# Kernel optimization log

Hardware: AMD Instinct MI355X
Metric: run time of the kernel (lower is better)

The kernel has to match this reference:

```python
import jax, jax.numpy as jnp
import numpy as np

T, D_IN, H, D_OUT = 20, 4, 768, 1
B = 1024


def setup_inputs() -> dict:
    key = jax.random.key(0)
    ks = jax.random.split(key, 8)
    s = 1.0 / np.sqrt(H)
    return {
        "batch_price": jax.random.normal(ks[0], (B, T, D_IN), jnp.float32),
        "batch_event": jax.random.normal(ks[1], (B, T, H), jnp.float32),
        "W_ih": jax.random.uniform(ks[2], (T, 4 * H, D_IN), jnp.float32, -s, s),
        "W_hh": jax.random.uniform(ks[3], (T, 4 * H, H), jnp.float32, -s, s),
        "b_ih": jax.random.uniform(ks[4], (T, 4 * H), jnp.float32, -s, s),
        "b_hh": jax.random.uniform(ks[5], (T, 4 * H), jnp.float32, -s, s),
        "fc_w": jax.random.uniform(ks[6], (D_OUT, H), jnp.float32, -s, s),
        "fc_b": jax.random.uniform(ks[7], (D_OUT,), jnp.float32, -s, s),
    }


def _lstm_cell(x, h_mat, c, wih, whh, bih, bhh):
    # gates: [B, 4H] in PyTorch LSTMCell order (i, f, g, o)
    gates = x @ wih.T + bih + h_mat @ whh.T + bhh
    i, f, g, o = jnp.split(gates, 4, axis=-1)
    c_next = jax.nn.sigmoid(f) * c + jax.nn.sigmoid(i) * jnp.tanh(g)
    h_next = jax.nn.sigmoid(o) * jnp.tanh(c_next)
    return h_next, c_next


def reference(batch_price, batch_event, W_ih, W_hh, b_ih, b_hh, fc_w, fc_b):
    Bb, Tt, _ = batch_price.shape
    Hh = W_hh.shape[-1]
    # step 0: hx = batch_event[:, 0], cell state = zeros
    h, c = _lstm_cell(batch_price[:, 0], batch_event[:, 0],
                      jnp.zeros((Bb, Hh), batch_price.dtype),
                      W_ih[0], W_hh[0], b_ih[0], b_hh[0])

    def step(carry, inp):
        h, c = carry
        x, ev, wih, whh, bih, bhh = inp
        # faithful to source: hx = torch.sum(batch_event_t + h_prev) -> scalar
        hx = jnp.sum(ev + h)
        h_mat = jnp.broadcast_to(hx, (Bb, Hh))
        h2, c2 = _lstm_cell(x, h_mat, c, wih, whh, bih, bhh)
        return (h2, c2), None

    xs = (jnp.swapaxes(batch_price[:, 1:], 0, 1),  # [T-1, B, D_IN]
          jnp.swapaxes(batch_event[:, 1:], 0, 1),  # [T-1, B, H]
          W_ih[1:], W_hh[1:], b_ih[1:], b_hh[1:])
    (h, c), _ = jax.lax.scan(step, (h, c), xs)
    return h @ fc_w.T + fc_b  # [B, 1]
```

## Files before the change

kernel.cpp:

```cpp
#include <hip/hip_runtime.h>
#include <stdint.h>

#define Bsz 1024
#define Tn  20
#define Hn  768
#define G4n 3072

#define WS_SH    0
#define WS_SEV   32
#define WS_PART  64
#define WS_BCAST 576
#define WS_RS    640
#define WS_BS    (640 + Tn*G4n)
#define WS_C     (640 + 2*Tn*G4n)

#define NB_GEMM   768
#define NB_ROWSUM 14592
#define NB_BIAS   240
#define NB_SEV    1216
#define NB_TOTAL  (NB_GEMM + NB_ROWSUM + NB_BIAS + NB_SEV)

typedef float  floatx4 __attribute__((ext_vector_type(4)));
typedef short  bfrag8  __attribute__((ext_vector_type(8)));

__device__ __forceinline__ float wave_reduce(float v){
#pragma unroll
    for (int o = 32; o > 0; o >>= 1) v += __shfl_down(v, o, 64);
    return v;
}
__device__ __forceinline__ float sigf(float x){ return 1.0f/(1.0f+__expf(-x)); }
__device__ __forceinline__ float tanhfast(float x){ return 2.0f/(1.0f+__expf(-2.0f*x)) - 1.0f; }
__device__ __forceinline__ unsigned short f2bf(float f){
    uint32_t u = __float_as_uint(f);
    return (unsigned short)((u + 0x7fffu + ((u>>16)&1u)) >> 16);
}
__device__ __forceinline__ float bf2f(unsigned short h){ return __uint_as_float(((uint32_t)h)<<16); }
__device__ __forceinline__ uint64_t pack_tv(unsigned t, float v){
    return ((uint64_t)t << 32) | (uint64_t)__float_as_uint(v);
}

__global__ void k_init(float* __restrict__ ws){
    if (threadIdx.x < 640) ws[threadIdx.x] = 0.0f;
}

__global__ __launch_bounds__(256) void k_pre(
    const float* __restrict__ price, const float* __restrict__ ev,
    const float* __restrict__ wih,   const float* __restrict__ whh,
    const float* __restrict__ bih,   const float* __restrict__ bhh,
    float* __restrict__ ws)
{
    __shared__ __align__(16) char smraw[4*64*56*2 + 16];
    unsigned short* Ah = (unsigned short*)smraw;
    unsigned short* Al = Ah + 64*56;
    unsigned short* Bh = Al + 64*56;
    unsigned short* Bl = Bh + 64*56;
    float* redk = (float*)(smraw + 4*64*56*2);
    float* red  = (float*)smraw;

    int blk = blockIdx.x, tid = threadIdx.x;

    if (blk < NB_GEMM) {
        float* Sh   = ws + WS_SH;
        float* cbuf = ws + WS_C;
        int bt = blk / 48, kt = blk % 48;
        int b0 = bt*64, k0 = kt*16;
        int w = tid >> 6, lane = tid & 63;
        int q = lane >> 4, col = lane & 15;

        int srow = tid >> 2;
        int kkoff = (tid & 3) * 8;
        int g_s = srow >> 4, rr = srow & 15;
        const float* aRow = ev  + (size_t)(b0 + srow)*(Tn*Hn);
        const float* bRow = whh + (size_t)(g_s*Hn + k0 + rr)*Hn;

        floatx4 acc[4];
#pragma unroll
        for (int g = 0; g < 4; ++g) acc[g] = (floatx4){0.f,0.f,0.f,0.f};

        for (int kk0 = 0; kk0 < Hn; kk0 += 32) {
            {
                const float* p = aRow + kk0 + kkoff;
                float4 v0 = *(const float4*)p;
                float4 v1 = *(const float4*)(p+4);
                float f[8] = {v0.x,v0.y,v0.z,v0.w,v1.x,v1.y,v1.z,v1.w};
                bfrag8 hv, lv;
#pragma unroll
                for (int i = 0; i < 8; ++i) {
                    unsigned short hb = f2bf(f[i]);
                    hv[i] = (short)hb;
                    lv[i] = (short)f2bf(f[i] - bf2f(hb));
                }
                *(bfrag8*)&Ah[srow*56 + kkoff] = hv;
                *(bfrag8*)&Al[srow*56 + kkoff] = lv;
                const float* pb = bRow + kk0 + kkoff;
                float4 u0 = *(const float4*)pb;
                float4 u1 = *(const float4*)(pb+4);
                float fb[8] = {u0.x,u0.y,u0.z,u0.w,u1.x,u1.y,u1.z,u1.w};
#pragma unroll
                for (int i = 0; i < 8; ++i) {
                    unsigned short hb = f2bf(fb[i]);
                    hv[i] = (short)hb;
                    lv[i] = (short)f2bf(fb[i] - bf2f(hb));
                }
                *(bfrag8*)&Bh[srow*56 + kkoff] = hv;
                *(bfrag8*)&Bl[srow*56 + kkoff] = lv;
            }
            __syncthreads();

            bfrag8 ah = *(const bfrag8*)&Ah[(w*16 + col)*56 + q*8];
            bfrag8 al = *(const bfrag8*)&Al[(w*16 + col)*56 + q*8];
#pragma unroll
            for (int g = 0; g < 4; ++g) {
                bfrag8 bh = *(const bfrag8*)&Bh[(g*16 + col)*56 + q*8];
                bfrag8 bl = *(const bfrag8*)&Bl[(g*16 + col)*56 + q*8];
                acc[g] = __builtin_amdgcn_mfma_f32_16x16x32_bf16(ah, bh, acc[g], 0,0,0);
                acc[g] = __builtin_amdgcn_mfma_f32_16x16x32_bf16(ah, bl, acc[g], 0,0,0);
                acc[g] = __builtin_amdgcn_mfma_f32_16x16x32_bf16(al, bh, acc[g], 0,0,0);
            }
            __syncthreads();
        }

        float hsum = 0.f;
#pragma unroll
        for (int r = 0; r < 4; ++r) {
            int b = b0 + w*16 + q*4 + r;
            float4 xv = *(const float4*)(price + (size_t)b*(Tn*4));
            float gates[4];
#pragma unroll
            for (int g = 0; g < 4; ++g) {
                int j = g*Hn + k0 + col;
                float4 wv = *(const float4*)(wih + (size_t)j*4);
                gates[g] = acc[g][r] + xv.x*wv.x + xv.y*wv.y + xv.z*wv.z + xv.w*wv.w
                         + bih[j] + bhh[j];
            }
            float c0 = sigf(gates[0]) * tanhfast(gates[2]);
            float h0 = sigf(gates[3]) * tanhfast(c0);
            cbuf[(size_t)b*Hn + k0 + col] = c0;
            hsum += h0;
        }
        hsum = wave_reduce(hsum);
        if (lane == 0) redk[w] = hsum;
        __syncthreads();
        if (tid == 0) atomicAdd(&Sh[0], redk[0]+redk[1]+redk[2]+redk[3]);
        return;
    }

    blk -= NB_GEMM;
    float* Sev     = ws + WS_SEV;
    float* rowsum  = ws + WS_RS;
    float* biassum = ws + WS_BS;

    if (blk < NB_ROWSUM) {
        int r    = blk*4 + (tid>>6);
        int lane = tid & 63;
        int t    = 1 + r/G4n;
        int j    = r - (t-1)*G4n;
        const float* base = whh + (size_t)t*G4n*Hn + (size_t)j*Hn;
        float s = 0.f;
#pragma unroll
        for (int i = 0; i < 3; ++i) {
            float4 v = *(const float4*)(base + (size_t)(lane + 64*i)*4);
            s += v.x + v.y + v.z + v.w;
        }
        s = wave_reduce(s);
        if (lane == 0) rowsum[t*G4n + j] = s;
    } else if (blk < NB_ROWSUM + NB_BIAS) {
        int idx = (blk - NB_ROWSUM)*256 + tid;
        if (idx < Tn*G4n) biassum[idx] = bih[idx] + bhh[idx];
    } else {
        int sb = blk - NB_ROWSUM - NB_BIAS;
        int t  = 1 + (sb >> 6);
        int b0 = (sb & 63) * 16;
        float s = 0.f;
        for (int bb = 0; bb < 16; ++bb) {
            const float* base = ev + (size_t)(b0+bb)*(Tn*Hn) + (size_t)t*Hn;
            s += base[tid] + base[tid+256] + base[tid+512];
        }
        s = wave_reduce(s);
        if ((tid & 63) == 0) red[tid>>6] = s;
        __syncthreads();
        if (tid == 0) atomicAdd(&Sev[t], red[0]+red[1]+red[2]+red[3]);
    }
}

__global__ __launch_bounds__(768) void k_steps(
    const float* __restrict__ price, const float* __restrict__ wih,
    const float* __restrict__ fcw,   const float* __restrict__ fcb,
    float* __restrict__ ws, float* __restrict__ out)
{
    __shared__ float pr[4][80];
    __shared__ float red[12];
    __shared__ float redP[4];
    __shared__ float redF[4][12];
    __shared__ float shx;

    float* Sh  = ws + WS_SH;
    float* Sev = ws + WS_SEV;
    uint64_t* part  = (uint64_t*)(ws + WS_PART);
    uint64_t* bcast = (uint64_t*)(ws + WS_BCAST);
    const float* rowsum  = ws + WS_RS;
    const float* biassum = ws + WS_BS;
    float* cbuf = ws + WS_C;

    int blk = blockIdx.x, tid = threadIdx.x;
    int lane = tid & 63, wid = tid >> 6;
    int k = tid;

    if (tid < 320) {
        int e = tid / 80, r = tid - e*80;
        pr[e][r] = price[(size_t)(blk + 256*e)*(Tn*4) + r];
    }

    float c[4];
#pragma unroll
    for (int e = 0; e < 4; ++e)
        c[e] = cbuf[(size_t)(blk + 256*e)*Hn + k];

    float fcwk = fcw[k];
    float fcb0 = fcb[0];

    float hsum_prev = 0.f;
    float vout[4] = {0.f,0.f,0.f,0.f};

    for (int t = 1; t < Tn; ++t) {
        const float* wih_t = wih + (size_t)t*G4n*4;
        float rsv[4], base[4][4];
#pragma unroll
        for (int g = 0; g < 4; ++g) {
            int j = g*Hn + k;
            float4 wv = *(const float4*)(wih_t + (size_t)j*4);
            rsv[g]   = rowsum[t*G4n + j];
            float bs = biassum[t*G4n + j];
#pragma unroll
            for (int e = 0; e < 4; ++e) {
                base[e][g] = pr[e][t*4+0]*wv.x + pr[e][t*4+1]*wv.y
                           + pr[e][t*4+2]*wv.z + pr[e][t*4+3]*wv.w + bs;
            }
        }

        if (t >= 2) {
            float v = wave_reduce(hsum_prev);
            if (lane == 0) red[wid] = v;
            __syncthreads();
            if (tid == 0) {
                float tot = 0.f;
#pragma unroll
                for (int i = 0; i < 12; ++i) tot += red[i];
                __hip_atomic_store(&part[blk], pack_tv((unsigned)(t-1), tot),
                                   __ATOMIC_RELAXED, __HIP_MEMORY_SCOPE_AGENT);
            }
        }

        if (blk == 0) {
            if (t >= 2) {
                if (tid < 256) {
                    uint64_t u;
                    do { u = __hip_atomic_load(&part[tid], __ATOMIC_RELAXED, __HIP_MEMORY_SCOPE_AGENT); }
                    while ((unsigned)(u >> 32) != (unsigned)(t-1));
                    float pv = wave_reduce(__uint_as_float((uint32_t)u));
                    if (lane == 0) redP[wid] = pv;
                }
                __syncthreads();
                if (tid == 0) {
                    float Shprev = redP[0]+redP[1]+redP[2]+redP[3];
                    float hx = Sev[t] + Shprev;
                    shx = hx;
                    __hip_atomic_store(bcast, pack_tv((unsigned)t, hx),
                                       __ATOMIC_RELAXED, __HIP_MEMORY_SCOPE_AGENT);
                }
            } else {
                if (tid == 0) {
                    float hx = Sev[1] + Sh[0];
                    shx = hx;
                    __hip_atomic_store(bcast, pack_tv(1u, hx),
                                       __ATOMIC_RELAXED, __HIP_MEMORY_SCOPE_AGENT);
                }
            }
            __syncthreads();
        } else {
            if (tid == 0) {
                uint64_t u;
                do { u = __hip_atomic_load(bcast, __ATOMIC_RELAXED, __HIP_MEMORY_SCOPE_AGENT); }
                while ((unsigned)(u >> 32) != (unsigned)t);
                shx = __uint_as_float((uint32_t)u);
            }
            __syncthreads();
        }
        float hx = shx;

        float hsum = 0.f;
#pragma unroll
        for (int e = 0; e < 4; ++e) {
            float gi = base[e][0] + hx*rsv[0];
            float gf = base[e][1] + hx*rsv[1];
            float gg = base[e][2] + hx*rsv[2];
            float go = base[e][3] + hx*rsv[3];
            float cn = sigf(gf)*c[e] + sigf(gi)*tanhfast(gg);
            c[e] = cn;
            float h = sigf(go)*tanhfast(cn);
            hsum += h;
            if (t == Tn-1) vout[e] = wave_reduce(h * fcwk);
        }
        hsum_prev = hsum;
    }

    if (lane == 0) {
#pragma unroll
        for (int e = 0; e < 4; ++e) redF[e][wid] = vout[e];
    }
    __syncthreads();
    if (tid < 4) {
        float tot = 0.f;
#pragma unroll
        for (int i = 0; i < 12; ++i) tot += redF[tid][i];
        out[blk + 256*tid] = tot + fcb0;
    }
}

extern "C" void kernel_launch(void* const* d_in, const int* in_sizes, int n_in,
                              void* d_out, int out_size, void* d_ws, size_t ws_size,
                              hipStream_t stream)
{
    const float* price = (const float*)d_in[0];
    const float* ev    = (const float*)d_in[1];
    const float* wih   = (const float*)d_in[2];
    const float* whh   = (const float*)d_in[3];
    const float* bih   = (const float*)d_in[4];
    const float* bhh   = (const float*)d_in[5];
    const float* fcw   = (const float*)d_in[6];
    const float* fcb   = (const float*)d_in[7];
    float* out = (float*)d_out;
    float* ws  = (float*)d_ws;

    k_init<<<1, 640, 0, stream>>>(ws);
    k_pre <<<NB_TOTAL, 256, 0, stream>>>(price, ev, wih, whh, bih, bhh, ws);
    k_steps<<<256, 768, 0, stream>>>(price, wih, fcw, fcb, ws, out);
}
```

Before: 416.4 us.

## Pre-split bf16 operands, skip forget gate, widen reductions, decentralize step sync

Adds a conversion kernel that splits the event slice and recurrent weights into bf16 hi/lo once, so the step-0 GEMM reads them straight from global memory without the LDS staging and syncthreads. That GEMM drops the forget-gate columns, since the initial cell state is zero. Row-sum and event-sum reductions each handle eight rows per wave with float4 loads, and the bias sum is vectorised. In the step kernel every block polls all partial sums directly, with a sleep, instead of waiting for block 0 to broadcast, which removes one global hop per step but adds polling traffic.

Result: slower. 475.2 us (+14.1%).

```diff
diff --git a/kernel.cpp b/kernel.cpp
--- a/kernel.cpp
+++ b/kernel.cpp
@@ -11,14 +11,23 @@
 #define WS_PART  64
 #define WS_BCAST 576
 #define WS_RS    640
-#define WS_BS    (640 + Tn*G4n)
-#define WS_C     (640 + 2*Tn*G4n)
+#define WS_BS    62080
+#define WS_C     123520
+#define WS_EVH   909952
+#define WS_EVL   1303168
+#define WS_WH    1696384
+#define WS_WL    2581120
+
+#define NBC_EV   512
+#define NBC_W    1152
+#define NBC_Z    3
+#define NBC_TOT  (NBC_EV + NBC_W + NBC_Z)
 
 #define NB_GEMM   768
-#define NB_ROWSUM 14592
-#define NB_BIAS   240
-#define NB_SEV    1216
-#define NB_TOTAL  (NB_GEMM + NB_ROWSUM + NB_BIAS + NB_SEV)
+#define NB_ROWSUM 1824
+#define NB_SEV    608
+#define NB_BIAS   60
+#define NB_TOTAL  (NB_GEMM + NB_ROWSUM + NB_SEV + NB_BIAS)
 
 typedef float  floatx4 __attribute__((ext_vector_type(4)));
 typedef short  bfrag8  __attribute__((ext_vector_type(8)));
@@ -39,8 +48,47 @@
     return ((uint64_t)t << 32) | (uint64_t)__float_as_uint(v);
 }
 
-__global__ void k_init(float* __restrict__ ws){
-    if (threadIdx.x < 640) ws[threadIdx.x] = 0.0f;
+__global__ __launch_bounds__(256) void k_conv(
+    const float* __restrict__ ev, const float* __restrict__ whh,
+    float* __restrict__ ws)
+{
+    int bid = blockIdx.x, tid = threadIdx.x;
+    if (bid < NBC_EV + NBC_W) {
+        if (tid >= 192) return;
+        int r = tid / 96;
+        int i = (tid - r*96) * 8;
+        const float* src;
+        unsigned short *dh, *dl;
+        if (bid < NBC_EV) {
+            int b = bid*2 + r;
+            src = ev + (size_t)b*(Tn*Hn) + i;
+            dh = (unsigned short*)(ws + WS_EVH) + (size_t)b*Hn + i;
+            dl = (unsigned short*)(ws + WS_EVL) + (size_t)b*Hn + i;
+        } else {
+            int p = (bid - NBC_EV)*2 + r;
+            int gsel = p / Hn;
+            int ga = (gsel==0) ? 0 : (gsel==1 ? 2 : 3);
+            int j = ga*Hn + (p - gsel*Hn);
+            src = whh + (size_t)j*Hn + i;
+            dh = (unsigned short*)(ws + WS_WH) + (size_t)p*Hn + i;
+            dl = (unsigned short*)(ws + WS_WL) + (size_t)p*Hn + i;
+        }
+        float4 v0 = *(const float4*)src;
+        float4 v1 = *(const float4*)(src+4);
+        float f[8] = {v0.x,v0.y,v0.z,v0.w,v1.x,v1.y,v1.z,v1.w};
+        bfrag8 hv, lv;
+#pragma unroll
+        for (int q = 0; q < 8; ++q) {
+            unsigned short hb = f2bf(f[q]);
+            hv[q] = (short)hb;
+            lv[q] = (short)f2bf(f[q] - bf2f(hb));
+        }
+        *(bfrag8*)dh = hv;
+        *(bfrag8*)dl = lv;
+    } else {
+        int idx = (bid - NBC_EV - NBC_W)*256 + tid;
+        if (idx < 640) ws[idx] = 0.0f;
+    }
 }
 
 __global__ __launch_bounds__(256) void k_pre(
@@ -49,75 +97,58 @@
     const float* __restrict__ bih,   const float* __restrict__ bhh,
     float* __restrict__ ws)
 {
-    __shared__ __align__(16) char smraw[4*64*56*2 + 16];
-    unsigned short* Ah = (unsigned short*)smraw;
-    unsigned short* Al = Ah + 64*56;
-    unsigned short* Bh = Al + 64*56;
-    unsigned short* Bl = Bh + 64*56;
-    float* redk = (float*)(smraw + 4*64*56*2);
-    float* red  = (float*)smraw;
-
+    __shared__ float redk[4];
     int blk = blockIdx.x, tid = threadIdx.x;
+    int lane = tid & 63, wid = tid >> 6;
 
     if (blk < NB_GEMM) {
         float* Sh   = ws + WS_SH;
         float* cbuf = ws + WS_C;
         int bt = blk / 48, kt = blk % 48;
         int b0 = bt*64, k0 = kt*16;
-        int w = tid >> 6, lane = tid & 63;
-        int q = lane >> 4, col = lane & 15;
-
-        int srow = tid >> 2;
-        int kkoff = (tid & 3) * 8;
-        int g_s = srow >> 4, rr = srow & 15;
-        const float* aRow = ev  + (size_t)(b0 + srow)*(Tn*Hn);
-        const float* bRow = whh + (size_t)(g_s*Hn + k0 + rr)*Hn;
-
-        floatx4 acc[4];
-#pragma unroll
-        for (int g = 0; g < 4; ++g) acc[g] = (floatx4){0.f,0.f,0.f,0.f};
-
-        for (int kk0 = 0; kk0 < Hn; kk0 += 32) {
-            {
-                const float* p = aRow + kk0 + kkoff;
-                float4 v0 = *(const float4*)p;
-                float4 v1 = *(const float4*)(p+4);
-                float f[8] = {v0.x,v0.y,v0.z,v0.w,v1.x,v1.y,v1.z,v1.w};
-                bfrag8 hv, lv;
-#pragma unroll
-                for (int i = 0; i < 8; ++i) {
-                    unsigned short hb = f2bf(f[i]);
-                    hv[i] = (short)hb;
-                    lv[i] = (short)f2bf(f[i] - bf2f(hb));
-                }
-                *(bfrag8*)&Ah[srow*56 + kkoff] = hv;
-                *(bfrag8*)&Al[srow*56 + kkoff] = lv;
-                const float* pb = bRow + kk0 + kkoff;
-                float4 u0 = *(const float4*)pb;
-                float4 u1 = *(const float4*)(pb+4);
-                float fb[8] = {u0.x,u0.y,u0.z,u0.w,u1.x,u1.y,u1.z,u1.w};
-#pragma unroll
-                for (int i = 0; i < 8; ++i) {
-                    unsigned short hb = f2bf(fb[i]);
-                    hv[i] = (short)hb;
-                    lv[i] = (short)f2bf(fb[i] - bf2f(hb));
-                }
-                *(bfrag8*)&Bh[srow*56 + kkoff] = hv;
-                *(bfrag8*)&Bl[srow*56 + kkoff] = lv;
-            }
-            __syncthreads();
-
-            bfrag8 ah = *(const bfrag8*)&Ah[(w*16 + col)*56 + q*8];
-            bfrag8 al = *(const bfrag8*)&Al[(w*16 + col)*56 + q*8];
-#pragma unroll
-            for (int g = 0; g < 4; ++g) {
-                bfrag8 bh = *(const bfrag8*)&Bh[(g*16 + col)*56 + q*8];
-                bfrag8 bl = *(const bfrag8*)&Bl[(g*16 + col)*56 + q*8];
-                acc[g] = __builtin_amdgcn_mfma_f32_16x16x32_bf16(ah, bh, acc[g], 0,0,0);
-                acc[g] = __builtin_amdgcn_mfma_f32_16x16x32_bf16(ah, bl, acc[g], 0,0,0);
-                acc[g] = __builtin_amdgcn_mfma_f32_16x16x32_bf16(al, bh, acc[g], 0,0,0);
-            }
-            __syncthreads();
+        int w = wid, q = lane >> 4, col = lane & 15;
+
+        const unsigned short* evh = (const unsigned short*)(ws + WS_EVH);
+        const unsigned short* evl = (const unsigned short*)(ws + WS_EVL);
+        const unsigned short* wh  = (const unsigned short*)(ws + WS_WH);
+        const unsigned short* wl  = (const unsigned short*)(ws + WS_WL);
+
+        int arow = b0 + w*16 + col;
+        const unsigned short* pah = evh + (size_t)arow*Hn + q*8;
+        const unsigned short* pal = evl + (size_t)arow*Hn + q*8;
+        int br0 = 0*Hn + k0 + col;
+        int br1 = 1*Hn + k0 + col;
+        int br2 = 2*Hn + k0 + col;
+        const unsigned short* pbh0 = wh + (size_t)br0*Hn + q*8;
+        const unsigned short* pbl0 = wl + (size_t)br0*Hn + q*8;
+        const unsigned short* pbh1 = wh + (size_t)br1*Hn + q*8;
+        const unsigned short* pbl1 = wl + (size_t)br1*Hn + q*8;
+        const unsigned short* pbh2 = wh + (size_t)br2*Hn + q*8;
+        const unsigned short* pbl2 = wl + (size_t)br2*Hn + q*8;
+
+        floatx4 acc0 = (floatx4){0.f,0.f,0.f,0.f};
+        floatx4 acc1 = (floatx4){0.f,0.f,0.f,0.f};
+        floatx4 acc2 = (floatx4){0.f,0.f,0.f,0.f};
+
+#pragma unroll 4
+        for (int kk = 0; kk < Hn; kk += 32) {
+            bfrag8 ah = *(const bfrag8*)(pah + kk);
+            bfrag8 al = *(const bfrag8*)(pal + kk);
+            bfrag8 b0h = *(const bfrag8*)(pbh0 + kk);
+            bfrag8 b0l = *(const bfrag8*)(pbl0 + kk);
+            acc0 = __builtin_amdgcn_mfma_f32_16x16x32_bf16(ah, b0h, acc0, 0,0,0);
+            acc0 = __builtin_amdgcn_mfma_f32_16x16x32_bf16(ah, b0l, acc0, 0,0,0);
+            acc0 = __builtin_amdgcn_mfma_f32_16x16x32_bf16(al, b0h, acc0, 0,0,0);
+            bfrag8 b1h = *(const bfrag8*)(pbh1 + kk);
+            bfrag8 b1l = *(const bfrag8*)(pbl1 + kk);
+            acc1 = __builtin_amdgcn_mfma_f32_16x16x32_bf16(ah, b1h, acc1, 0,0,0);
+            acc1 = __builtin_amdgcn_mfma_f32_16x16x32_bf16(ah, b1l, acc1, 0,0,0);
+            acc1 = __builtin_amdgcn_mfma_f32_16x16x32_bf16(al, b1h, acc1, 0,0,0);
+            bfrag8 b2h = *(const bfrag8*)(pbh2 + kk);
+            bfrag8 b2l = *(const bfrag8*)(pbl2 + kk);
+            acc2 = __builtin_amdgcn_mfma_f32_16x16x32_bf16(ah, b2h, acc2, 0,0,0);
+            acc2 = __builtin_amdgcn_mfma_f32_16x16x32_bf16(ah, b2l, acc2, 0,0,0);
+            acc2 = __builtin_amdgcn_mfma_f32_16x16x32_bf16(al, b2h, acc2, 0,0,0);
         }
 
         float hsum = 0.f;
@@ -125,16 +156,17 @@
         for (int r = 0; r < 4; ++r) {
             int b = b0 + w*16 + q*4 + r;
             float4 xv = *(const float4*)(price + (size_t)b*(Tn*4));
-            float gates[4];
-#pragma unroll
-            for (int g = 0; g < 4; ++g) {
-                int j = g*Hn + k0 + col;
-                float4 wv = *(const float4*)(wih + (size_t)j*4);
-                gates[g] = acc[g][r] + xv.x*wv.x + xv.y*wv.y + xv.z*wv.z + xv.w*wv.w
-                         + bih[j] + bhh[j];
-            }
-            float c0 = sigf(gates[0]) * tanhfast(gates[2]);
-            float h0 = sigf(gates[3]) * tanhfast(c0);
+            int j0 = 0*Hn + k0 + col;
+            int j1 = 2*Hn + k0 + col;
+            int j2 = 3*Hn + k0 + col;
+            float4 w0 = *(const float4*)(wih + (size_t)j0*4);
+            float4 w1 = *(const float4*)(wih + (size_t)j1*4);
+            float4 w2 = *(const float4*)(wih + (size_t)j2*4);
+            float gi = acc0[r] + xv.x*w0.x + xv.y*w0.y + xv.z*w0.z + xv.w*w0.w + bih[j0] + bhh[j0];
+            float gg = acc1[r] + xv.x*w1.x + xv.y*w1.y + xv.z*w1.z + xv.w*w1.w + bih[j1] + bhh[j1];
+            float go = acc2[r] + xv.x*w2.x + xv.y*w2.y + xv.z*w2.z + xv.w*w2.w + bih[j2] + bhh[j2];
+            float c0 = sigf(gi) * tanhfast(gg);
+            float h0 = sigf(go) * tanhfast(c0);
             cbuf[(size_t)b*Hn + k0 + col] = c0;
             hsum += h0;
         }
@@ -146,40 +178,54 @@
     }
 
     blk -= NB_GEMM;
-    float* Sev     = ws + WS_SEV;
-    float* rowsum  = ws + WS_RS;
-    float* biassum = ws + WS_BS;
-
     if (blk < NB_ROWSUM) {
-        int r    = blk*4 + (tid>>6);
-        int lane = tid & 63;
-        int t    = 1 + r/G4n;
-        int j    = r - (t-1)*G4n;
-        const float* base = whh + (size_t)t*G4n*Hn + (size_t)j*Hn;
+        int gw = blk*4 + wid;
+        int t  = 1 + gw/384;
+        int j0 = (gw - (t-1)*384)*8;
+        const float* base = whh + ((size_t)t*G4n + j0)*Hn + (size_t)lane*4;
+        float s[8];
+#pragma unroll
+        for (int r = 0; r < 8; ++r) {
+            float4 v0 = *(const float4*)(base + (size_t)r*Hn);
+            float4 v1 = *(const float4*)(base + (size_t)r*Hn + 256);
+            float4 v2 = *(const float4*)(base + (size_t)r*Hn + 512);
+            s[r] = (v0.x+v0.y+v0.z+v0.w) + (v1.x+v1.y+v1.z+v1.w) + (v2.x+v2.y+v2.z+v2.w);
+        }
+        float* rowsum = ws + WS_RS;
+#pragma unroll
+        for (int r = 0; r < 8; ++r) {
+            float rs = wave_reduce(s[r]);
+            if (lane == 0) rowsum[(size_t)t*G4n + j0 + r] = rs;
+        }
+        return;
+    }
+
+    blk -= NB_ROWSUM;
+    if (blk < NB_SEV) {
+        int gw = blk*4 + wid;
+        int t   = 1 + gw/128;
+        int b0s = (gw - (t-1)*128)*8;
         float s = 0.f;
 #pragma unroll
-        for (int i = 0; i < 3; ++i) {
-            float4 v = *(const float4*)(base + (size_t)(lane + 64*i)*4);
-            s += v.x + v.y + v.z + v.w;
+        for (int r = 0; r < 8; ++r) {
+            const float* base = ev + ((size_t)(b0s+r)*Tn + t)*Hn + (size_t)lane*4;
+            float4 v0 = *(const float4*)(base);
+            float4 v1 = *(const float4*)(base + 256);
+            float4 v2 = *(const float4*)(base + 512);
+            s += (v0.x+v0.y+v0.z+v0.w) + (v1.x+v1.y+v1.z+v1.w) + (v2.x+v2.y+v2.z+v2.w);
         }
         s = wave_reduce(s);
-        if (lane == 0) rowsum[t*G4n + j] = s;
-    } else if (blk < NB_ROWSUM + NB_BIAS) {
-        int idx = (blk - NB_ROWSUM)*256 + tid;
-        if (idx < Tn*G4n) biassum[idx] = bih[idx] + bhh[idx];
-    } else {
-        int sb = blk - NB_ROWSUM - NB_BIAS;
-        int t  = 1 + (sb >> 6);
-        int b0 = (sb & 63) * 16;
-        float s = 0.f;
-        for (int bb = 0; bb < 16; ++bb) {
-            const float* base = ev + (size_t)(b0+bb)*(Tn*Hn) + (size_t)t*Hn;
-            s += base[tid] + base[tid+256] + base[tid+512];
-        }
-        s = wave_reduce(s);
-        if ((tid & 63) == 0) red[tid>>6] = s;
-        __syncthreads();
-        if (tid == 0) atomicAdd(&Sev[t], red[0]+red[1]+red[2]+red[3]);
+        if (lane == 0) atomicAdd(ws + WS_SEV + t, s);
+        return;
+    }
+
+    blk -= NB_SEV;
+    {
+        int idx = blk*256 + tid;
+        float4 a = *(const float4*)(bih + (size_t)idx*4);
+        float4 b = *(const float4*)(bhh + (size_t)idx*4);
+        float4 r4; r4.x=a.x+b.x; r4.y=a.y+b.y; r4.z=a.z+b.z; r4.w=a.w+b.w;
+        *(float4*)(ws + WS_BS + (size_t)idx*4) = r4;
     }
 }
 
@@ -192,12 +238,10 @@
     __shared__ float red[12];
     __shared__ float redP[4];
     __shared__ float redF[4][12];
-    __shared__ float shx;
 
     float* Sh  = ws + WS_SH;
     float* Sev = ws + WS_SEV;
-    uint64_t* part  = (uint64_t*)(ws + WS_PART);
-    uint64_t* bcast = (uint64_t*)(ws + WS_BCAST);
+    uint64_t* part = (uint64_t*)(ws + WS_PART);
     const float* rowsum  = ws + WS_RS;
     const float* biassum = ws + WS_BS;
     float* cbuf = ws + WS_C;
@@ -218,26 +262,14 @@
 
     float fcwk = fcw[k];
     float fcb0 = fcb[0];
+    float sh0  = Sh[0];
+
+    __syncthreads();
 
     float hsum_prev = 0.f;
     float vout[4] = {0.f,0.f,0.f,0.f};
 
     for (int t = 1; t < Tn; ++t) {
-        const float* wih_t = wih + (size_t)t*G4n*4;
-        float rsv[4], base[4][4];
-#pragma unroll
-        for (int g = 0; g < 4; ++g) {
-            int j = g*Hn + k;
-            float4 wv = *(const float4*)(wih_t + (size_t)j*4);
-            rsv[g]   = rowsum[t*G4n + j];
-            float bs = biassum[t*G4n + j];
-#pragma unroll
-            for (int e = 0; e < 4; ++e) {
-                base[e][g] = pr[e][t*4+0]*wv.x + pr[e][t*4+1]*wv.y
-                           + pr[e][t*4+2]*wv.z + pr[e][t*4+3]*wv.w + bs;
-            }
-        }
-
         if (t >= 2) {
             float v = wave_reduce(hsum_prev);
             if (lane == 0) red[wid] = v;
@@ -251,42 +283,38 @@
             }
         }
 
-        if (blk == 0) {
-            if (t >= 2) {
-                if (tid < 256) {
-                    uint64_t u;
-                    do { u = __hip_atomic_load(&part[tid], __ATOMIC_RELAXED, __HIP_MEMORY_SCOPE_AGENT); }
-                    while ((unsigned)(u >> 32) != (unsigned)(t-1));
-                    float pv = wave_reduce(__uint_as_float((uint32_t)u));
-                    if (lane == 0) redP[wid] = pv;
+        const float* wih_t = wih + (size_t)t*G4n*4;
+        float rsv[4], base[4][4];
+#pragma unroll
+        for (int g = 0; g < 4; ++g) {
+            int j = g*Hn + k;
+            float4 wv = *(const float4*)(wih_t + (size_t)j*4);
+            rsv[g]   = rowsum[t*G4n + j];
+            float bs = biassum[t*G4n + j];
+#pragma unroll
+            for (int e = 0; e < 4; ++e) {
+                base[e][g] = pr[e][t*4+0]*wv.x + pr[e][t*4+1]*wv.y
+                           + pr[e][t*4+2]*wv.z + pr[e][t*4+3]*wv.w + bs;
+            }
+        }
+        float sevt = Sev[t];
+
+        float hx;
+        if (t == 1) {
+            hx = sevt + sh0;
+        } else {
+            if (tid < 256) {
+                uint64_t u = __hip_atomic_load(&part[tid], __ATOMIC_RELAXED, __HIP_MEMORY_SCOPE_AGENT);
+                while ((unsigned)(u >> 32) != (unsigned)(t-1)) {
+                    __builtin_amdgcn_s_sleep(1);
+                    u = __hip_atomic_load(&part[tid], __ATOMIC_RELAXED, __HIP_MEMORY_SCOPE_AGENT);
                 }
-                __syncthreads();
-                if (tid == 0) {
-                    float Shprev = redP[0]+redP[1]+redP[2]+redP[3];
-                    float hx = Sev[t] + Shprev;
-                    shx = hx;
-                    __hip_atomic_store(bcast, pack_tv((unsigned)t, hx),
-                                       __ATOMIC_RELAXED, __HIP_MEMORY_SCOPE_AGENT);
-                }
-            } else {
-                if (tid == 0) {
-                    float hx = Sev[1] + Sh[0];
-                    shx = hx;
-                    __hip_atomic_store(bcast, pack_tv(1u, hx),
-                                       __ATOMIC_RELAXED, __HIP_MEMORY_SCOPE_AGENT);
-                }
+                float pv = wave_reduce(__uint_as_float((uint32_t)u));
+                if (lane == 0) redP[wid] = pv;
             }
             __syncthreads();
-        } else {
-            if (tid == 0) {
-                uint64_t u;
-                do { u = __hip_atomic_load(bcast, __ATOMIC_RELAXED, __HIP_MEMORY_SCOPE_AGENT); }
-                while ((unsigned)(u >> 32) != (unsigned)t);
-                shx = __uint_as_float((uint32_t)u);
-            }
-            __syncthreads();
-        }
-        float hx = shx;
+            hx = sevt + (redP[0]+redP[1]+redP[2]+redP[3]);
+        }
 
         float hsum = 0.f;
 #pragma unroll
@@ -332,7 +360,7 @@
     float* out = (float*)d_out;
     float* ws  = (float*)d_ws;
 
-    k_init<<<1, 640, 0, stream>>>(ws);
-    k_pre <<<NB_TOTAL, 256, 0, stream>>>(price, ev, wih, whh, bih, bhh, ws);
+    k_conv <<<NBC_TOT, 256, 0, stream>>>(ev, whh, ws);
+    k_pre  <<<NB_TOTAL, 256, 0, stream>>>(price, ev, wih, whh, bih, bhh, ws);
     k_steps<<<256, 768, 0, stream>>>(price, wih, fcw, fcb, ws, out);
 }
```
